# Kernel tuning notes

Measured on AMD Instinct MI355X. Metric: run time of the kernel, lower is better.

## Reference

```python
import jax, jax.numpy as jnp
import numpy as np

B, S, DIM = 2, 2048, 2048
H, KVH, HD = 16, 4, 128
WIN = 512
ROPE_BASE = 10000.0
EPS = 1.1920928955078125e-07  # torch F.rms_norm default eps for fp32


def setup_inputs() -> dict:
    key = jax.random.key(0)
    ks = jax.random.split(key, 6)
    kv_dim = KVH * HD
    sc = lambda fan_in: 1.0 / np.sqrt(fan_in)
    return {
        "x": jax.random.normal(ks[0], (B, S, DIM), jnp.float32),
        "Wq": jax.random.normal(ks[1], (DIM, DIM), jnp.float32) * sc(DIM),
        "Wk": jax.random.normal(ks[2], (kv_dim, DIM), jnp.float32) * sc(DIM),
        "Wv": jax.random.normal(ks[3], (kv_dim, DIM), jnp.float32) * sc(DIM),
        "Wo": jax.random.normal(ks[4], (DIM, DIM), jnp.float32) * sc(DIM),
        "q_gain": jnp.ones((H,), jnp.float32),
    }


def _rms_norm(x):
    return x * jax.lax.rsqrt(jnp.mean(x * x, axis=-1, keepdims=True) + EPS)


def _rope_tables(seqlen, dtype):
    half = HD // 2
    inv_freq = ROPE_BASE ** (-jnp.arange(0, half, dtype=jnp.float32) / half)
    freqs = jnp.arange(seqlen, dtype=jnp.float32)[:, None] * inv_freq[None, :]  # [S, HD/2]
    return jnp.cos(freqs).astype(dtype), jnp.sin(freqs).astype(dtype)


def _apply_rotary(x, cos, sin):
    # x: [B, H, S, HD]; cos/sin: [S, HD/2]
    half = x.shape[-1] // 2
    x1, x2 = x[..., :half], x[..., half:]
    c = cos[None, None, :, :]
    s = sin[None, None, :, :]
    return jnp.concatenate([x1 * c + x2 * s, -x1 * s + x2 * c], axis=-1)


def reference(x, Wq, Wk, Wv, Wo, q_gain):
    bsz, seqlen, dim = x.shape
    q = jnp.einsum("bsd,ed->bse", x, Wq).reshape(bsz, seqlen, H, HD).transpose(0, 2, 1, 3)
    k = jnp.einsum("bsd,ed->bse", x, Wk).reshape(bsz, seqlen, KVH, HD).transpose(0, 2, 1, 3)
    v = jnp.einsum("bsd,ed->bse", x, Wv).reshape(bsz, seqlen, KVH, HD).transpose(0, 2, 1, 3)

    q = _rms_norm(q)
    k = _rms_norm(k)

    cos, sin = _rope_tables(seqlen, q.dtype)
    q = _apply_rotary(q, cos, sin)
    k = _apply_rotary(k, cos, sin)

    q = q * q_gain[None, :, None, None]

    # GQA: expand kv heads to match query heads
    rep = H // KVH
    k = jnp.repeat(k, rep, axis=1)
    v = jnp.repeat(v, rep, axis=1)

    row = jnp.arange(seqlen)[:, None]
    col = jnp.arange(seqlen)[None, :]
    mask = (col <= row) & (col >= row - WIN + 1)  # [S, S]

    scale = 1.0 / np.sqrt(HD)
    scores = jnp.einsum("bhsd,bhtd->bhst", q, k) * scale
    scores = jnp.where(mask[None, None, :, :], scores, -jnp.inf)
    attn = jax.nn.softmax(scores, axis=-1)
    y = jnp.einsum("bhst,bhtd->bhsd", attn, v)  # [B, H, S, HD]

    y = y.transpose(0, 2, 1, 3).reshape(bsz, seqlen, dim)
    return jnp.einsum("bsd,ed->bse", y, Wo)
```

## Files before the change

### kernel.cpp

```cpp
#include <hip/hip_runtime.h>

#define S_LEN 2048
#define DIM   2048
#define NH    16
#define NKV   4
#define HD    128
#define WIN   512
#define BATCH 2

typedef __bf16 bf16x8 __attribute__((ext_vector_type(8)));
typedef __bf16 bf16x4 __attribute__((ext_vector_type(4)));
typedef float  f32x4  __attribute__((ext_vector_type(4)));

union U8 { bf16x8 v; bf16x4 h[2]; };

__device__ inline void async_load16(const void* g, void* l) {
  __builtin_amdgcn_global_load_lds(
      (const __attribute__((address_space(1))) unsigned int*)g,
      (__attribute__((address_space(3))) unsigned int*)l, 16, 0, 0);
}

__global__ __launch_bounds__(256) void preprocess_kernel(
    const float* __restrict__ x,
    const float* __restrict__ Wq, const float* __restrict__ Wk,
    const float* __restrict__ Wv, const float* __restrict__ Wo,
    __bf16* __restrict__ xb, __bf16* __restrict__ wqkv, __bf16* __restrict__ wob,
    float* __restrict__ cosT, float* __restrict__ sinT) {
  const int blk = blockIdx.x, tid = threadIdx.x;
  if (blk < 8192) {
    int i = blk * 256 + tid;
    float4 v = ((const float4*)x)[i];
    bf16x4 o;
    o[0] = (__bf16)v.x; o[1] = (__bf16)v.y; o[2] = (__bf16)v.z; o[3] = (__bf16)v.w;
    ((bf16x4*)xb)[i] = o;
  } else if (blk < 18432) {
    int i = (blk - 8192) * 256 + tid;
    int orow = i >> 9, c = i & 511;
    const float* src;
    __bf16* dst;
    long soff;
    if (orow < 2048) {
      int n = orow & 127;
      int sr = (orow & ~127) + ((n >> 5) << 4) + (n & 15) + (((n >> 4) & 1) << 6);
      src = Wq; soff = (long)sr * 512 + c; dst = wqkv + (long)orow * 2048;
    } else if (orow < 2560) {
      int lr = orow - 2048, n = lr & 127;
      int sr = (lr & ~127) + ((n >> 5) << 4) + (n & 15) + (((n >> 4) & 1) << 6);
      src = Wk; soff = (long)sr * 512 + c; dst = wqkv + (long)orow * 2048;
    } else if (orow < 3072) {
      src = Wv; soff = (long)(orow - 2560) * 512 + c; dst = wqkv + (long)orow * 2048;
    } else {
      src = Wo; soff = (long)(orow - 3072) * 512 + c; dst = wob + (long)(orow - 3072) * 2048;
    }
    float4 v = ((const float4*)src)[soff];
    bf16x4 o;
    o[0] = (__bf16)v.x; o[1] = (__bf16)v.y; o[2] = (__bf16)v.z; o[3] = (__bf16)v.w;
    ((bf16x4*)dst)[c] = o;
  } else {
    int idx = (blk - 18432) * 256 + tid;
    int s = idx >> 6, d = idx & 63;
    float f = (float)s * powf(10000.f, -(float)d * (1.f / 64.f));
    float sn, cs;
    sincosf(f, &sn, &cs);
    cosT[idx] = cs;
    sinT[idx] = sn;
  }
}

__global__ __launch_bounds__(512, 2) void gemm_bt(
    const __bf16* __restrict__ A, const __bf16* __restrict__ Bt,
    float* __restrict__ C, int M, int N, int K) {
  extern __shared__ char smem[];
  const int NT = K >> 6;
  const int t = threadIdx.x;
  const int wid = t >> 6, lane = t & 63;
  const int quad = lane >> 4, l15 = lane & 15;
  const int wr = wid >> 2, wc = wid & 3;
  const long m0 = (long)blockIdx.x * 128, n0 = (long)blockIdx.y * 256;

  const int srw = (wid << 3) + (lane >> 3);
  const int c8 = (lane & 7) ^ ((lane >> 3) & 7);
  const __bf16* ag = A + (m0 + srw) * (long)K + c8 * 8;
  const __bf16* bg = Bt + (n0 + srw) * (long)K + c8 * 8;

  auto stageA = [&](int buf, int j, int kt) {
    async_load16(ag + (long)(j << 6) * K + (long)kt * 64,
                 smem + buf * 49152 + j * 8192 + t * 16);
  };
  auto stageB = [&](int buf, int j, int kt) {
    async_load16(bg + (long)(j << 6) * K + (long)kt * 64,
                 smem + buf * 49152 + 16384 + j * 8192 + t * 16);
  };

  const int swz = (l15 & 7) << 4;
  const int col0 = (quad * 16) ^ swz;
  const int col1 = (64 + quad * 16) ^ swz;

  f32x4 zero = {0.f, 0.f, 0.f, 0.f};
  f32x4 acc[4][4];
#pragma unroll
  for (int i = 0; i < 4; ++i)
#pragma unroll
    for (int j = 0; j < 4; ++j) acc[i][j] = zero;

#pragma unroll
  for (int j = 0; j < 2; ++j) stageA(0, j, 0);
#pragma unroll
  for (int j = 0; j < 4; ++j) stageB(0, j, 0);
#pragma unroll
  for (int j = 0; j < 2; ++j) stageA(1, j, 1);

  auto tile = [&](const int buf, const int tt) {
    const char* As = smem + buf * 49152;
    const char* Bs = smem + buf * 49152 + 16384;
    if (tt + 1 < NT) {
#pragma unroll
      for (int j = 0; j < 4; ++j) stageB(buf ^ 1, j, tt + 1);
      asm volatile("s_waitcnt vmcnt(6)" ::: "memory");
    } else {
      asm volatile("s_waitcnt vmcnt(0)" ::: "memory");
    }
    __builtin_amdgcn_s_barrier();
    bf16x8 af[4][2], bf[2][2];
#pragma unroll
    for (int i = 0; i < 4; ++i) {
      const int rb = (wr * 64 + i * 16 + l15) * 128;
      af[i][0] = *(const bf16x8*)(As + rb + col0);
      af[i][1] = *(const bf16x8*)(As + rb + col1);
    }
#pragma unroll
    for (int j = 0; j < 2; ++j) {
      const int rb = (wc * 64 + j * 16 + l15) * 128;
      bf[j][0] = *(const bf16x8*)(Bs + rb + col0);
      bf[j][1] = *(const bf16x8*)(Bs + rb + col1);
    }
    asm volatile("s_waitcnt lgkmcnt(0)" ::: "memory");
    __builtin_amdgcn_sched_barrier(0);
    __builtin_amdgcn_s_setprio(1);
#pragma unroll
    for (int kk = 0; kk < 2; ++kk)
#pragma unroll
      for (int i = 0; i < 4; ++i)
#pragma unroll
        for (int j = 0; j < 2; ++j)
          acc[i][j] = __builtin_amdgcn_mfma_f32_16x16x32_bf16(af[i][kk], bf[j][kk],
                                                              acc[i][j], 0, 0, 0);
    __builtin_amdgcn_s_setprio(0);
    __builtin_amdgcn_s_barrier();
#pragma unroll
    for (int j = 0; j < 2; ++j) {
      const int rb = (wc * 64 + (j + 2) * 16 + l15) * 128;
      bf[j][0] = *(const bf16x8*)(Bs + rb + col0);
      bf[j][1] = *(const bf16x8*)(Bs + rb + col1);
    }
    if (tt + 2 < NT) {
#pragma unroll
      for (int j = 0; j < 2; ++j) stageA(buf, j, tt + 2);
    }
    asm volatile("s_waitcnt lgkmcnt(0)" ::: "memory");
    __builtin_amdgcn_sched_barrier(0);
    __builtin_amdgcn_s_setprio(1);
#pragma unroll
    for (int kk = 0; kk < 2; ++kk)
#pragma unroll
      for (int i = 0; i < 4; ++i)
#pragma unroll
        for (int j = 0; j < 2; ++j)
          acc[i][j + 2] = __builtin_amdgcn_mfma_f32_16x16x32_bf16(af[i][kk], bf[j][kk],
                                                                  acc[i][j + 2], 0, 0, 0);
    __builtin_amdgcn_s_setprio(0);
    __builtin_amdgcn_s_barrier();
  };

  for (int tt = 0; tt < NT; tt += 2) {
    tile(0, tt);
    tile(1, tt + 1);
  }

#pragma unroll
  for (int i = 0; i < 4; ++i)
#pragma unroll
    for (int j = 0; j < 4; ++j)
#pragma unroll
      for (int r = 0; r < 4; ++r)
        C[(m0 + wr * 64 + i * 16 + quad * 4 + r) * (long)N + n0 + wc * 64 + j * 16 + l15] =
            acc[i][j][r];
}

__global__ __launch_bounds__(256) void gemm_qkv(
    const __bf16* __restrict__ A, const __bf16* __restrict__ Bt,
    const float* __restrict__ gain,
    const float* __restrict__ cosT, const float* __restrict__ sinT,
    __bf16* __restrict__ Qo, __bf16* __restrict__ Ko, __bf16* __restrict__ Vt) {
  __shared__ __bf16 As[128 * 32];
  __shared__ __bf16 Bs[128 * 32];
  const int K = 2048;
  const int t = threadIdx.x;
  const int wid = t >> 6, lane = t & 63;
  const int quad = lane >> 4, l15 = lane & 15;
  const long m0 = (long)blockIdx.x * 128, n0 = (long)blockIdx.y * 128;
  const int wm = (wid >> 1) * 64, wn = (wid & 1) * 64;

  const __bf16* ga = A + (m0 + (t >> 2)) * (long)K + (t & 3) * 8;
  const __bf16* gb = Bt + (n0 + (t >> 2)) * (long)K + (t & 3) * 8;
  char* lA = (char*)As + wid * 1024;
  char* lB = (char*)Bs + wid * 1024;
  const long rstride = 64L * K;

  f32x4 zero = {0.f, 0.f, 0.f, 0.f};
  f32x4 acc[4][4];
#pragma unroll
  for (int i = 0; i < 4; ++i)
#pragma unroll
    for (int j = 0; j < 4; ++j) acc[i][j] = zero;

  for (int k0 = 0; k0 < K; k0 += 32) {
    async_load16(ga + k0, lA);
    async_load16(ga + k0 + rstride, lA + 4096);
    async_load16(gb + k0, lB);
    async_load16(gb + k0 + rstride, lB + 4096);
    __syncthreads();
    bf16x8 af[4], bfr[4];
#pragma unroll
    for (int i = 0; i < 4; ++i) {
      af[i] = *(const bf16x8*)(As + (wm + i * 16 + l15) * 32 + quad * 8);
      bfr[i] = *(const bf16x8*)(Bs + (wn + i * 16 + l15) * 32 + quad * 8);
    }
#pragma unroll
    for (int i = 0; i < 4; ++i)
#pragma unroll
      for (int j = 0; j < 4; ++j)
        acc[i][j] = __builtin_amdgcn_mfma_f32_16x16x32_bf16(af[i], bfr[j], acc[i][j], 0, 0, 0);
    __syncthreads();
  }

  const int by = blockIdx.y;
  const int srow0 = (int)(m0 & 2047);
  const int bb = (int)(m0 >> 11);

  if (by >= 20) {
    const int kvh = by - 20;
    __bf16* Vb = Vt + ((long)(bb * NKV + kvh)) * HD * S_LEN;
#pragma unroll
    for (int i = 0; i < 4; ++i)
#pragma unroll
      for (int j = 0; j < 4; ++j) {
        int d = wn + j * 16 + l15;
        int s0 = srow0 + wm + i * 16 + quad * 4;
        bf16x4 o;
#pragma unroll
        for (int r = 0; r < 4; ++r) o[r] = (__bf16)acc[i][j][r];
        *(bf16x4*)(Vb + (long)d * S_LEN + s0) = o;
      }
  } else {
    float* sums = (float*)As;
#pragma unroll
    for (int i = 0; i < 4; ++i)
#pragma unroll
      for (int r = 0; r < 4; ++r) {
        float t2 = acc[i][0][r] * acc[i][0][r] + acc[i][1][r] * acc[i][1][r] +
                   acc[i][2][r] * acc[i][2][r] + acc[i][3][r] * acc[i][3][r];
#pragma unroll
        for (int off = 1; off < 16; off <<= 1) t2 += __shfl_xor(t2, off, 64);
        if (l15 == 0) sums[(wm + i * 16 + quad * 4 + r) * 2 + (wn >> 6)] = t2;
      }
    __syncthreads();

    float g;
    __bf16* base;
    if (by < 16) {
      g = gain[by] * 0.08838834764831845f;
      base = Qo + ((long)(bb * NH + by)) * S_LEN * HD;
    } else {
      g = 1.f;
      base = Ko + ((long)(bb * NKV + (by - 16))) * S_LEN * HD;
    }
#pragma unroll
    for (int i = 0; i < 4; ++i)
#pragma unroll
      for (int r = 0; r < 4; ++r) {
        int lrow = wm + i * 16 + quad * 4 + r;
        int srow = srow0 + lrow;
        float rs = rsqrtf((sums[lrow * 2] + sums[lrow * 2 + 1]) * (1.f / 128.f) +
                          1.1920928955078125e-07f);
#pragma unroll
        for (int a = 0; a < 2; ++a) {
          int dlow = (wn >> 1) + a * 16 + l15;
          float cv = cosT[srow * 64 + dlow];
          float sv = sinT[srow * 64 + dlow];
          float x1 = acc[i][2 * a][r] * rs;
          float x2 = acc[i][2 * a + 1][r] * rs;
          base[(long)srow * HD + wn + (2 * a) * 16 + l15] = (__bf16)((x1 * cv + x2 * sv) * g);
          base[(long)srow * HD + wn + (2 * a + 1) * 16 + l15] = (__bf16)((-x1 * sv + x2 * cv) * g);
        }
      }
  }
}

__global__ __launch_bounds__(512, 4) void attn_kernel(
    const __bf16* __restrict__ Q,
    const __bf16* __restrict__ K,
    const __bf16* __restrict__ Vt,
    const float* __restrict__ gain,
    __bf16* __restrict__ Y) {
  __shared__ __bf16 Ks[64 * 128];
  __shared__ __bf16 Vs[128 * 64];
  __shared__ __bf16 Ps[8][16 * 64];

  const int t = threadIdx.x;
  const int wid = t >> 6, lane = t & 63;
  const int quad = lane >> 4, l15 = lane & 15;
  const int qt_blk = 15 - blockIdx.x;
  const int h = blockIdx.y, b = blockIdx.z;
  const int kv = h >> 2;
  const int t0 = qt_blk * 128;
  const int r0 = t0 + wid * 16;

  const __bf16* Qb = Q + ((long)(b * NH + h)) * S_LEN * HD;
  const __bf16* Kb = K + ((long)(b * NKV + kv)) * S_LEN * HD;
  const __bf16* Vb = Vt + ((long)(b * NKV + kv)) * HD * S_LEN;
  const float M = 11.3137085f * fabsf(gain[h]);

  bf16x8 qf[4];
#pragma unroll
  for (int c = 0; c < 4; ++c)
    qf[c] = *(const bf16x8*)(Qb + (long)(r0 + l15) * HD + c * 32 + quad * 8);

  f32x4 zero = {0.f, 0.f, 0.f, 0.f};
  f32x4 acc[8];
#pragma unroll
  for (int d = 0; d < 8; ++d) acc[d] = zero;
  float lac = 0.f;

  int ksrc[2], vsrc[2];
#pragma unroll
  for (int j = 0; j < 2; ++j) {
    int kr = j * 32 + (t >> 4);
    ksrc[j] = kr * HD + (((t & 15) ^ (kr & 15)) << 3);
    int vd = j * 64 + (t >> 3);
    vsrc[j] = vd * S_LEN + (((t & 7) ^ (vd & 7)) << 3);
  }

  const int kstart = (t0 >= WIN) ? (t0 - WIN) : 0;
  const int ntiles = (t0 + 128 - kstart) >> 6;

  for (int it = 0; it < ntiles; ++it) {
    const int kt = kstart + it * 64;
#pragma unroll
    for (int j = 0; j < 2; ++j) {
      async_load16(Kb + (long)kt * HD + ksrc[j], (char*)Ks + j * 8192 + t * 16);
      async_load16(Vb + kt + vsrc[j], (char*)Vs + j * 8192 + t * 16);
    }
    __syncthreads();

    if (kt <= r0 + 15 && kt + 63 >= r0 - (WIN - 1)) {
#pragma unroll
      for (int kti = 0; kti < 4; ++kti) {
        bf16x8 kf[4];
#pragma unroll
        for (int c = 0; c < 4; ++c)
          kf[c] = *(const bf16x8*)(Ks + (kti * 16 + l15) * 128 +
                                   ((((c << 2) + quad) ^ l15) << 3));
        f32x4 sc = zero;
#pragma unroll
        for (int c = 0; c < 4; ++c)
          sc = __builtin_amdgcn_mfma_f32_16x16x32_bf16(kf[c], qf[c], sc, 0, 0, 0);
        const int qg = r0 + l15;
        const int kbase = kt + kti * 16 + quad * 4;
        bf16x4 pv;
#pragma unroll
        for (int r = 0; r < 4; ++r) {
          int key = kbase + r;
          float p = (key <= qg && key >= qg - (WIN - 1)) ? __expf(sc[r] - M) : 0.f;
          lac += p;
          pv[r] = (__bf16)p;
        }
        const int cb = kti * 4 + quad;
        *(bf16x4*)(&Ps[wid][l15 * 64 + ((cb ^ l15) << 2)]) = pv;
      }
      bf16x8 pf[2];
#pragma unroll
      for (int kc = 0; kc < 2; ++kc) {
        U8 u;
        u.h[0] = *(const bf16x4*)(&Ps[wid][l15 * 64 + (((kc * 8 + quad * 2) ^ l15) << 2)]);
        u.h[1] = *(const bf16x4*)(&Ps[wid][l15 * 64 + (((kc * 8 + quad * 2 + 1) ^ l15) << 2)]);
        pf[kc] = u.v;
      }
#pragma unroll
      for (int dt = 0; dt < 8; ++dt)
#pragma unroll
        for (int kc = 0; kc < 2; ++kc) {
          bf16x8 vf = *(const bf16x8*)(Vs + (dt * 16 + l15) * 64 +
                                       ((((kc << 2) + quad) ^ (l15 & 7)) << 3));
          acc[dt] = __builtin_amdgcn_mfma_f32_16x16x32_bf16(pf[kc], vf, acc[dt], 0, 0, 0);
        }
    }
    __syncthreads();
  }

  float s = lac;
  s += __shfl_xor(s, 16, 64);
  s += __shfl_xor(s, 32, 64);
  __bf16* Yb = Y + ((long)b * S_LEN) * DIM + h * HD;
#pragma unroll
  for (int r = 0; r < 4; ++r) {
    const int row = quad * 4 + r;
    float il = 1.f / __shfl(s, row, 64);
#pragma unroll
    for (int dt = 0; dt < 8; ++dt)
      Yb[(long)(r0 + row) * DIM + dt * 16 + l15] = (__bf16)(acc[dt][r] * il);
  }
}

extern "C" void kernel_launch(void* const* d_in, const int* in_sizes, int n_in,
                              void* d_out, int out_size, void* d_ws, size_t ws_size,
                              hipStream_t stream) {
  (void)in_sizes; (void)n_in; (void)out_size; (void)ws_size;
  const float* x  = (const float*)d_in[0];
  const float* Wq = (const float*)d_in[1];
  const float* Wk = (const float*)d_in[2];
  const float* Wv = (const float*)d_in[3];
  const float* Wo = (const float*)d_in[4];
  const float* qg = (const float*)d_in[5];
  float* out = (float*)d_out;

  char* ws = (char*)d_ws;
  size_t off = 0;
  auto alloc = [&](size_t bytes) -> void* {
    void* p = ws + off;
    off += (bytes + 255) & ~(size_t)255;
    return p;
  };
  __bf16* xb   = (__bf16*)alloc(8388608ull * 2);
  __bf16* wqkv = (__bf16*)alloc(3072ull * 2048 * 2);
  __bf16* wob  = (__bf16*)alloc(2048ull * 2048 * 2);
  __bf16* qo   = (__bf16*)alloc((size_t)BATCH * NH * S_LEN * HD * 2);
  __bf16* ko   = (__bf16*)alloc((size_t)BATCH * NKV * S_LEN * HD * 2);
  __bf16* vt   = (__bf16*)alloc((size_t)BATCH * NKV * HD * S_LEN * 2);
  float*  cosT = (float*)alloc(2048ull * 64 * 4);
  float*  sinT = (float*)alloc(2048ull * 64 * 4);
  __bf16* yb   = xb;

  (void)hipFuncSetAttribute((const void*)gemm_bt,
                            hipFuncAttributeMaxDynamicSharedMemorySize, 98304);

  preprocess_kernel<<<18944, 256, 0, stream>>>(x, Wq, Wk, Wv, Wo, xb, wqkv, wob,
                                               cosT, sinT);
  gemm_qkv<<<dim3(32, 24), 256, 0, stream>>>(xb, wqkv, qg, cosT, sinT, qo, ko, vt);
  attn_kernel<<<dim3(16, 16, 2), 512, 0, stream>>>(qo, ko, vt, qg, yb);
  gemm_bt<<<dim3(32, 8), 512, 98304, stream>>>(yb, wob, out, 4096, 2048, 2048);
}
```

Baseline: 240.6 us.

## Restructure QKV GEMM into 128x256 tiles with double-buffered swizzled LDS pipeline

The fused QKV projection GEMM moves from a 128x128 tile with 256 threads and single-buffered K=32 steps to a 128x256 tile with 512 threads. Each step now covers K=64, with double-buffered B tiles, XOR-swizzled LDS layout, and async prefetch of the next tile overlapped with MFMA work. It mirrors the pipelined structure already used in the output-projection GEMM. The epilogue is remapped so each block covers two heads, which adds LDS use (80KB dynamic) and more complex head indexing in the RMSNorm/RoPE epilogue.

```diff
diff --git a/kernel.cpp b/kernel.cpp
--- a/kernel.cpp
+++ b/kernel.cpp
@@ -187,25 +187,38 @@
             acc[i][j][r];
 }
 
-__global__ __launch_bounds__(256) void gemm_qkv(
+__global__ __launch_bounds__(512, 4) void gemm_qkv(
     const __bf16* __restrict__ A, const __bf16* __restrict__ Bt,
     const float* __restrict__ gain,
     const float* __restrict__ cosT, const float* __restrict__ sinT,
     __bf16* __restrict__ Qo, __bf16* __restrict__ Ko, __bf16* __restrict__ Vt) {
-  __shared__ __bf16 As[128 * 32];
-  __shared__ __bf16 Bs[128 * 32];
-  const int K = 2048;
+  extern __shared__ char smem[];
+  constexpr int K = 2048;
+  constexpr int NT = 32;
   const int t = threadIdx.x;
   const int wid = t >> 6, lane = t & 63;
   const int quad = lane >> 4, l15 = lane & 15;
-  const long m0 = (long)blockIdx.x * 128, n0 = (long)blockIdx.y * 128;
-  const int wm = (wid >> 1) * 64, wn = (wid & 1) * 64;
-
-  const __bf16* ga = A + (m0 + (t >> 2)) * (long)K + (t & 3) * 8;
-  const __bf16* gb = Bt + (n0 + (t >> 2)) * (long)K + (t & 3) * 8;
-  char* lA = (char*)As + wid * 1024;
-  char* lB = (char*)Bs + wid * 1024;
-  const long rstride = 64L * K;
+  const int wr = wid >> 2, wc = wid & 3;
+  const long m0 = (long)blockIdx.x * 128;
+  const long n0 = (long)blockIdx.y * 256;
+
+  const int srw = (wid << 3) + (lane >> 3);
+  const int c8 = (lane & 7) ^ ((lane >> 3) & 7);
+  const __bf16* ag = A + (m0 + srw) * (long)K + c8 * 8;
+  const __bf16* bg = Bt + (n0 + srw) * (long)K + c8 * 8;
+
+  auto stageA = [&](int j, int kt) {
+    async_load16(ag + (long)(j << 6) * K + (long)kt * 64,
+                 smem + j * 8192 + t * 16);
+  };
+  auto stageB = [&](int buf, int j, int kt) {
+    async_load16(bg + (long)(j << 6) * K + (long)kt * 64,
+                 smem + 16384 + buf * 32768 + j * 8192 + t * 16);
+  };
+
+  const int swz = (l15 & 7) << 4;
+  const int col0 = (quad * 16) ^ swz;
+  const int col1 = (64 + quad * 16) ^ swz;
 
   f32x4 zero = {0.f, 0.f, 0.f, 0.f};
   f32x4 acc[4][4];
@@ -214,46 +227,99 @@
 #pragma unroll
     for (int j = 0; j < 4; ++j) acc[i][j] = zero;
 
-  for (int k0 = 0; k0 < K; k0 += 32) {
-    async_load16(ga + k0, lA);
-    async_load16(ga + k0 + rstride, lA + 4096);
-    async_load16(gb + k0, lB);
-    async_load16(gb + k0 + rstride, lB + 4096);
-    __syncthreads();
-    bf16x8 af[4], bfr[4];
+#pragma unroll
+  for (int j = 0; j < 4; ++j) stageB(0, j, 0);
+#pragma unroll
+  for (int j = 0; j < 2; ++j) stageA(j, 0);
+
+  auto tile = [&](const int buf, const int tt) {
+    const char* As = smem;
+    const char* Bs = smem + 16384 + buf * 32768;
+    if (tt + 1 < NT) {
+#pragma unroll
+      for (int j = 0; j < 4; ++j) stageB(buf ^ 1, j, tt + 1);
+      asm volatile("s_waitcnt vmcnt(4)" ::: "memory");
+    } else {
+      asm volatile("s_waitcnt vmcnt(0)" ::: "memory");
+    }
+    __builtin_amdgcn_s_barrier();
+    bf16x8 af[4][2], bf[2][2];
 #pragma unroll
     for (int i = 0; i < 4; ++i) {
-      af[i] = *(const bf16x8*)(As + (wm + i * 16 + l15) * 32 + quad * 8);
-      bfr[i] = *(const bf16x8*)(Bs + (wn + i * 16 + l15) * 32 + quad * 8);
-    }
-#pragma unroll
-    for (int i = 0; i < 4; ++i)
-#pragma unroll
-      for (int j = 0; j < 4; ++j)
-        acc[i][j] = __builtin_amdgcn_mfma_f32_16x16x32_bf16(af[i], bfr[j], acc[i][j], 0, 0, 0);
-    __syncthreads();
+      const int rb = (wr * 64 + i * 16 + l15) * 128;
+      af[i][0] = *(const bf16x8*)(As + rb + col0);
+      af[i][1] = *(const bf16x8*)(As + rb + col1);
+    }
+#pragma unroll
+    for (int j = 0; j < 2; ++j) {
+      const int rb = (wc * 64 + j * 16 + l15) * 128;
+      bf[j][0] = *(const bf16x8*)(Bs + rb + col0);
+      bf[j][1] = *(const bf16x8*)(Bs + rb + col1);
+    }
+    asm volatile("s_waitcnt lgkmcnt(0)" ::: "memory");
+    __builtin_amdgcn_sched_barrier(0);
+    __builtin_amdgcn_s_setprio(1);
+#pragma unroll
+    for (int kk = 0; kk < 2; ++kk)
+#pragma unroll
+      for (int i = 0; i < 4; ++i)
+#pragma unroll
+        for (int j = 0; j < 2; ++j)
+          acc[i][j] = __builtin_amdgcn_mfma_f32_16x16x32_bf16(af[i][kk], bf[j][kk],
+                                                              acc[i][j], 0, 0, 0);
+    __builtin_amdgcn_s_setprio(0);
+    __builtin_amdgcn_s_barrier();
+    if (tt + 1 < NT) {
+#pragma unroll
+      for (int j = 0; j < 2; ++j) stageA(j, tt + 1);
+    }
+#pragma unroll
+    for (int j = 0; j < 2; ++j) {
+      const int rb = (wc * 64 + (j + 2) * 16 + l15) * 128;
+      bf[j][0] = *(const bf16x8*)(Bs + rb + col0);
+      bf[j][1] = *(const bf16x8*)(Bs + rb + col1);
+    }
+    asm volatile("s_waitcnt lgkmcnt(0)" ::: "memory");
+    __builtin_amdgcn_sched_barrier(0);
+    __builtin_amdgcn_s_setprio(1);
+#pragma unroll
+    for (int kk = 0; kk < 2; ++kk)
+#pragma unroll
+      for (int i = 0; i < 4; ++i)
+#pragma unroll
+        for (int j = 0; j < 2; ++j)
+          acc[i][j + 2] = __builtin_amdgcn_mfma_f32_16x16x32_bf16(af[i][kk], bf[j][kk],
+                                                                  acc[i][j + 2], 0, 0, 0);
+    __builtin_amdgcn_s_setprio(0);
+    __builtin_amdgcn_s_barrier();
+  };
+
+  for (int tt = 0; tt < NT; tt += 2) {
+    tile(0, tt);
+    tile(1, tt + 1);
   }
 
   const int by = blockIdx.y;
   const int srow0 = (int)(m0 & 2047);
   const int bb = (int)(m0 >> 11);
-
-  if (by >= 20) {
-    const int kvh = by - 20;
+  const int brow = (wc & 1) << 6;
+
+  if (by >= 10) {
+    const int kvh = (by - 10) * 2 + (wc >> 1);
     __bf16* Vb = Vt + ((long)(bb * NKV + kvh)) * HD * S_LEN;
 #pragma unroll
     for (int i = 0; i < 4; ++i)
 #pragma unroll
       for (int j = 0; j < 4; ++j) {
-        int d = wn + j * 16 + l15;
-        int s0 = srow0 + wm + i * 16 + quad * 4;
+        const int d = brow + j * 16 + l15;
+        const int s0 = srow0 + wr * 64 + i * 16 + quad * 4;
         bf16x4 o;
 #pragma unroll
         for (int r = 0; r < 4; ++r) o[r] = (__bf16)acc[i][j][r];
         *(bf16x4*)(Vb + (long)d * S_LEN + s0) = o;
       }
   } else {
-    float* sums = (float*)As;
+    float* sums = (float*)smem;
 #pragma unroll
     for (int i = 0; i < 4; ++i)
 #pragma unroll
@@ -262,36 +328,39 @@
                    acc[i][2][r] * acc[i][2][r] + acc[i][3][r] * acc[i][3][r];
 #pragma unroll
         for (int off = 1; off < 16; off <<= 1) t2 += __shfl_xor(t2, off, 64);
-        if (l15 == 0) sums[(wm + i * 16 + quad * 4 + r) * 2 + (wn >> 6)] = t2;
+        if (l15 == 0) sums[(wr * 64 + i * 16 + quad * 4 + r) * 4 + wc] = t2;
       }
     __syncthreads();
 
     float g;
     __bf16* base;
-    if (by < 16) {
-      g = gain[by] * 0.08838834764831845f;
-      base = Qo + ((long)(bb * NH + by)) * S_LEN * HD;
+    if (by < 8) {
+      const int h = by * 2 + (wc >> 1);
+      g = gain[h] * 0.08838834764831845f;
+      base = Qo + ((long)(bb * NH + h)) * S_LEN * HD;
     } else {
+      const int h = (by - 8) * 2 + (wc >> 1);
       g = 1.f;
-      base = Ko + ((long)(bb * NKV + (by - 16))) * S_LEN * HD;
+      base = Ko + ((long)(bb * NKV + h)) * S_LEN * HD;
     }
 #pragma unroll
     for (int i = 0; i < 4; ++i)
 #pragma unroll
       for (int r = 0; r < 4; ++r) {
-        int lrow = wm + i * 16 + quad * 4 + r;
-        int srow = srow0 + lrow;
-        float rs = rsqrtf((sums[lrow * 2] + sums[lrow * 2 + 1]) * (1.f / 128.f) +
-                          1.1920928955078125e-07f);
+        const int lrow = wr * 64 + i * 16 + quad * 4 + r;
+        const int srow = srow0 + lrow;
+        const float rs = rsqrtf((sums[lrow * 4 + (wc & 2)] + sums[lrow * 4 + (wc & 2) + 1]) *
+                                    (1.f / 128.f) +
+                                1.1920928955078125e-07f);
 #pragma unroll
         for (int a = 0; a < 2; ++a) {
-          int dlow = (wn >> 1) + a * 16 + l15;
-          float cv = cosT[srow * 64 + dlow];
-          float sv = sinT[srow * 64 + dlow];
-          float x1 = acc[i][2 * a][r] * rs;
-          float x2 = acc[i][2 * a + 1][r] * rs;
-          base[(long)srow * HD + wn + (2 * a) * 16 + l15] = (__bf16)((x1 * cv + x2 * sv) * g);
-          base[(long)srow * HD + wn + (2 * a + 1) * 16 + l15] = (__bf16)((-x1 * sv + x2 * cv) * g);
+          const int dlow = ((wc & 1) << 5) + a * 16 + l15;
+          const float cv = cosT[srow * 64 + dlow];
+          const float sv = sinT[srow * 64 + dlow];
+          const float x1 = acc[i][2 * a][r] * rs;
+          const float x2 = acc[i][2 * a + 1][r] * rs;
+          base[(long)srow * HD + brow + (2 * a) * 16 + l15] = (__bf16)((x1 * cv + x2 * sv) * g);
+          base[(long)srow * HD + brow + (2 * a + 1) * 16 + l15] = (__bf16)((-x1 * sv + x2 * cv) * g);
         }
       }
   }
@@ -443,10 +512,12 @@
 
   (void)hipFuncSetAttribute((const void*)gemm_bt,
                             hipFuncAttributeMaxDynamicSharedMemorySize, 98304);
+  (void)hipFuncSetAttribute((const void*)gemm_qkv,
+                            hipFuncAttributeMaxDynamicSharedMemorySize, 81920);
 
   preprocess_kernel<<<18944, 256, 0, stream>>>(x, Wq, Wk, Wv, Wo, xb, wqkv, wob,
                                                cosT, sinT);
-  gemm_qkv<<<dim3(32, 24), 256, 0, stream>>>(xb, wqkv, qg, cosT, sinT, qo, ko, vt);
+  gemm_qkv<<<dim3(32, 12), 512, 81920, stream>>>(xb, wqkv, qg, cosT, sinT, qo, ko, vt);
   attn_kernel<<<dim3(16, 16, 2), 512, 0, stream>>>(qo, ko, vt, qg, yb);
   gemm_bt<<<dim3(32, 8), 512, 98304, stream>>>(yb, wob, out, 4096, 2048, 2048);
 }
```

Result: slower. 345.1 us (+43.4%).
